# Optimization experiments

Hardware: AMD Instinct MI355X
Metric: run time of the kernel (lower is better)

## Reference

```python
import jax, jax.numpy as jnp
import numpy as np

N_EMBD = 256
HEAD_SIZE = 64


def setup_inputs() -> dict:
    key = jax.random.key(0)
    ks = jax.random.split(key, 6)
    B, T = 4, 4096
    x = jax.random.normal(ks[0], (B, T, N_EMBD), dtype=jnp.float32)
    s = 1.0 / np.sqrt(N_EMBD)
    Wk = jax.random.normal(ks[1], (N_EMBD, HEAD_SIZE), dtype=jnp.float32) * s
    bk = jax.random.normal(ks[2], (HEAD_SIZE,), dtype=jnp.float32) * s
    Wq = jax.random.normal(ks[3], (N_EMBD, HEAD_SIZE), dtype=jnp.float32) * s
    bq = jax.random.normal(ks[4], (HEAD_SIZE,), dtype=jnp.float32) * s
    Wv = jax.random.normal(ks[5], (N_EMBD, HEAD_SIZE), dtype=jnp.float32) * s
    return {"x": x, "Wk": Wk, "bk": bk, "Wq": Wq, "bq": bq, "Wv": Wv}


def reference(x, Wk, bk, Wq, bq, Wv):
    # x: [B, T, C] with C = n_embd = 256
    C = x.shape[-1]
    k = x @ Wk + bk          # [B, T, H]
    q = x @ Wq + bq          # [B, T, H]
    v = x @ Wv               # [B, T, H] (no bias)
    # NOTE: original scales by C**-0.5 (n_embd), not head_size**-0.5
    scale = jnp.asarray(C, x.dtype) ** -0.5
    wei = jnp.einsum("bth,bsh->bts", q, k) * scale   # [B, T, T]
    wei = jax.nn.softmax(wei, axis=-1)
    # dropout on attention weights is identity in eval mode
    out = jnp.einsum("bts,bsh->bth", wei, v)         # [B, T, H]
    return out
```

## Files before the change

### kernel.cpp

```cpp
#include <hip/hip_runtime.h>
#include <stdint.h>

#define QK_SCALE 0.09016844005555021f

typedef short short8 __attribute__((ext_vector_type(8)));
typedef float f32x4 __attribute__((ext_vector_type(4)));

static __device__ __forceinline__ unsigned short f2bf(float f){
  unsigned u = __builtin_bit_cast(unsigned, f);
  u += 0x7fffu + ((u >> 16) & 1u);
  return (unsigned short)(u >> 16);
}
static __device__ __forceinline__ float fexp2(float x){
  float r; asm("v_exp_f32 %0, %1" : "=v"(r) : "v"(x)); return r;
}
static __device__ __forceinline__ unsigned cvtpk(float lo, float hi){
  unsigned r; asm("v_cvt_pk_bf16_f32 %0, %1, %2" : "=v"(r) : "v"(lo), "v"(hi));
  return r;
}

__global__ __launch_bounds__(256) void pack_w_k(const float* __restrict__ Wk,
    const float* __restrict__ Wq, const float* __restrict__ Wv,
    unsigned short* __restrict__ wt){
  int j = blockIdx.x >> 6;
  int n = blockIdx.x & 63;
  int k = threadIdx.x;
  const float* W = (j==0) ? Wk : ((j==1) ? Wq : Wv);
  float s = (j==1) ? QK_SCALE : 1.0f;
  wt[j*16384 + n*256 + k] = f2bf(W[k*64 + n] * s);
}

__global__ __launch_bounds__(256) void qkv_proj_k(const float* __restrict__ x,
    const float* __restrict__ bk, const float* __restrict__ bq,
    const unsigned short* __restrict__ wt,
    unsigned short* __restrict__ qw, unsigned short* __restrict__ kw,
    unsigned short* __restrict__ vtw){
  __shared__ __align__(16) unsigned char xl[8192];
  __shared__ __align__(16) unsigned short vb[16*72];
  const int tid = threadIdx.x;
  const int r0 = blockIdx.x << 4;

  #pragma unroll
  for (int i=0;i<4;++i){
    int f4 = tid + (i<<8);
    float4 v = ((const float4*)x)[((size_t)r0<<6) + f4];
    int row = f4 >> 6;
    int byt = ((row<<9) + ((f4&63)<<3)) ^ ((row&7)<<4);
    uint2 pk; pk.x = cvtpk(v.x, v.y); pk.y = cvtpk(v.z, v.w);
    *(uint2*)(xl + byt) = pk;
  }
  __syncthreads();

  const int l = tid & 63, w = tid >> 6, g = l >> 4, c = l & 15;
  const int jn0 = w * 3;
  f32x4 acc[3];
  #pragma unroll
  for (int i=0;i<3;++i) acc[i] = (f32x4){0.f,0.f,0.f,0.f};

  #pragma unroll
  for (int kk=0;kk<8;++kk){
    short8 a = *(const short8*)(xl + (((c<<9) + (kk<<6) + (g<<4)) ^ ((c&7)<<4)));
    #pragma unroll
    for (int u=0;u<3;++u){
      int jn = jn0 + u, j = jn>>2, n = jn&3;
      short8 bf = *(const short8*)(wt + (size_t)j*16384 + (((n<<4)+c)<<8) + (kk<<5) + (g<<3));
      acc[u] = __builtin_amdgcn_mfma_f32_16x16x32_bf16(a, bf, acc[u], 0, 0, 0);
    }
  }

  #pragma unroll
  for (int u=0;u<3;++u){
    int jn = jn0 + u, j = jn>>2, n = jn&3;
    if (j == 0){
      float bK = bk[(n<<4)+c];
      #pragma unroll
      for (int r=0;r<4;++r)
        kw[((size_t)(r0 + (g<<2) + r)<<6) + (n<<4) + c] = f2bf(acc[u][r] + bK);
    } else if (j == 1){
      float bQ = bq[(n<<4)+c] * QK_SCALE;
      #pragma unroll
      for (int r=0;r<4;++r)
        qw[((size_t)(r0 + (g<<2) + r)<<6) + (n<<4) + c] = f2bf(acc[u][r] + bQ);
    } else {
      #pragma unroll
      for (int r=0;r<4;++r)
        vb[((g<<2)+r)*72 + (n<<4) + c] = f2bf(acc[u][r]);
    }
  }
  __syncthreads();
  int d = tid >> 2, tq = (tid & 3) << 2;
  unsigned s0 = vb[(tq+0)*72 + d], s1 = vb[(tq+1)*72 + d];
  unsigned s2 = vb[(tq+2)*72 + d], s3 = vb[(tq+3)*72 + d];
  uint2 pk; pk.x = s0 | (s1<<16); pk.y = s2 | (s3<<16);
  int b = r0 >> 12, t0 = r0 & 4095;
  *(uint2*)(vtw + (((size_t)(b<<6) + d)<<12) + t0 + tq) = pk;
}

__global__ __launch_bounds__(256) void attn_k(
    const unsigned short* __restrict__ qw, const unsigned short* __restrict__ kw,
    const unsigned short* __restrict__ vtw,
    float* __restrict__ opart, float* __restrict__ mpart, float* __restrict__ lpart){
  __shared__ __align__(16) unsigned char kl[16384];
  __shared__ __align__(16) unsigned char vl[16384];
  const int tid = threadIdx.x;
  const int l = tid & 63, w = tid >> 6, g = l >> 4, c = l & 15;
  const int qb = blockIdx.x, split = blockIdx.y;
  const int b = qb >> 5, tq0 = (qb & 31) << 7;
  const int kt0 = split << 3;

  short8 qa[2][2];
  #pragma unroll
  for (int mt=0;mt<2;++mt)
    #pragma unroll
    for (int kk=0;kk<2;++kk)
      qa[mt][kk] = *(const short8*)(qw +
        ((size_t)((b<<12) + tq0 + (w<<5) + (mt<<4) + c)<<6) + (kk<<5) + (g<<3));

  f32x4 o[2][4];
  float mrow[2] = {-1e30f, -1e30f}, lrow[2] = {0.f, 0.f};
  #pragma unroll
  for (int mt=0;mt<2;++mt)
    #pragma unroll
    for (int df=0;df<4;++df) o[mt][df] = (f32x4){0.f,0.f,0.f,0.f};

  const int srow = tid >> 3;
  const int scol = tid & 7;
  const int offA = ((scol>>2)<<6) + ((scol&1)<<5) + (((scol>>1)&1)<<3);
  const int offB = offA + 16;

  uint4 rk[2], rv[2];
  #define LOADT(kt) { \
    _Pragma("unroll") \
    for (int u=0;u<2;++u){ \
      int row = srow + (u<<5); \
      rk[u] = *(const uint4*)(kw + ((size_t)((b<<12) + ((kt)<<6) + row)<<6) + (scol<<3)); \
      rv[u] = *(const uint4*)(vtw + (((size_t)((b<<6) + row))<<12) + ((kt)<<6) + (scol<<3)); \
    } }
  #define STORET(buf) { \
    _Pragma("unroll") \
    for (int u=0;u<2;++u){ \
      int row = srow + (u<<5); \
      *(uint4*)(kl + ((buf)<<13) + (((row<<7)+(scol<<4)) ^ ((row&7)<<4))) = rk[u]; \
      unsigned char* vbase = vl + ((buf)<<13) + (row<<7); \
      int sz = (row&7)<<4; \
      uint2 t0_; t0_.x = rv[u].x; t0_.y = rv[u].y; \
      uint2 t1_; t1_.x = rv[u].z; t1_.y = rv[u].w; \
      *(uint2*)(vbase + (offA ^ sz)) = t0_; \
      *(uint2*)(vbase + (offB ^ sz)) = t1_; \
    } }

  LOADT(kt0); STORET(0);
  __syncthreads();

  for (int it=0; it<8; ++it){
    const int buf = it & 1;
    if (it < 7) LOADT(kt0 + it + 1);
    const unsigned char* kb_ = kl + (buf<<13);
    const unsigned char* vb_ = vl + (buf<<13);

    f32x4 s[2][4];
    #pragma unroll
    for (int mt=0;mt<2;++mt)
      #pragma unroll
      for (int n=0;n<4;++n) s[mt][n] = (f32x4){0.f,0.f,0.f,0.f};
    __builtin_amdgcn_s_setprio(1);
    #pragma unroll
    for (int kk=0;kk<2;++kk){
      #pragma unroll
      for (int n=0;n<4;++n){
        int rowk = (n<<4) + c;
        short8 ka = *(const short8*)(kb_ + (((rowk<<7) + (kk<<6) + (g<<4)) ^ ((rowk&7)<<4)));
        s[0][n] = __builtin_amdgcn_mfma_f32_16x16x32_bf16(ka, qa[0][kk], s[0][n], 0,0,0);
        s[1][n] = __builtin_amdgcn_mfma_f32_16x16x32_bf16(ka, qa[1][kk], s[1][n], 0,0,0);
      }
    }
    __builtin_amdgcn_s_setprio(0);

    short8 pb[2][2];
    #pragma unroll
    for (int mt=0;mt<2;++mt){
      float a0 = fmaxf(fmaxf(s[mt][0][0], s[mt][0][1]), fmaxf(s[mt][0][2], s[mt][0][3]));
      float a1 = fmaxf(fmaxf(s[mt][1][0], s[mt][1][1]), fmaxf(s[mt][1][2], s[mt][1][3]));
      float a2 = fmaxf(fmaxf(s[mt][2][0], s[mt][2][1]), fmaxf(s[mt][2][2], s[mt][2][3]));
      float a3 = fmaxf(fmaxf(s[mt][3][0], s[mt][3][1]), fmaxf(s[mt][3][2], s[mt][3][3]));
      float t0 = fmaxf(fmaxf(a0,a1), fmaxf(a2,a3));
      t0 = fmaxf(t0, __shfl_xor(t0, 16));
      t0 = fmaxf(t0, __shfl_xor(t0, 32));
      float mo = mrow[mt];
      if (!__all(t0 <= mo + 8.f)){
        float mn = fmaxf(mo, t0);
        float al = fexp2(mo - mn);
        mrow[mt] = mn; lrow[mt] *= al;
        #pragma unroll
        for (int df=0;df<4;++df){
          o[mt][df][0]*=al; o[mt][df][1]*=al; o[mt][df][2]*=al; o[mt][df][3]*=al;
        }
      }
      float m = mrow[mt];
      #pragma unroll
      for (int n=0;n<4;++n)
        #pragma unroll
        for (int r=0;r<4;++r) s[mt][n][r] = fexp2(s[mt][n][r] - m);
      float p0 = (s[mt][0][0]+s[mt][0][1]) + (s[mt][0][2]+s[mt][0][3]);
      float p1 = (s[mt][1][0]+s[mt][1][1]) + (s[mt][1][2]+s[mt][1][3]);
      float p2 = (s[mt][2][0]+s[mt][2][1]) + (s[mt][2][2]+s[mt][2][3]);
      float p3 = (s[mt][3][0]+s[mt][3][1]) + (s[mt][3][2]+s[mt][3][3]);
      lrow[mt] += (p0+p1) + (p2+p3);
      #pragma unroll
      for (int kk=0;kk<2;++kk){
        uint4 pw;
        pw.x = cvtpk(s[mt][2*kk][0],   s[mt][2*kk][1]);
        pw.y = cvtpk(s[mt][2*kk][2],   s[mt][2*kk][3]);
        pw.z = cvtpk(s[mt][2*kk+1][0], s[mt][2*kk+1][1]);
        pw.w = cvtpk(s[mt][2*kk+1][2], s[mt][2*kk+1][3]);
        pb[mt][kk] = __builtin_bit_cast(short8, pw);
      }
    }

    __builtin_amdgcn_s_setprio(1);
    #pragma unroll
    for (int kk=0;kk<2;++kk){
      #pragma unroll
      for (int df=0;df<4;++df){
        int rowd = (df<<4) + c;
        short8 va = *(const short8*)(vb_ + (((rowd<<7) + (kk<<6) + (g<<4)) ^ ((rowd&7)<<4)));
        o[0][df] = __builtin_amdgcn_mfma_f32_16x16x32_bf16(va, pb[0][kk], o[0][df], 0,0,0);
        o[1][df] = __builtin_amdgcn_mfma_f32_16x16x32_bf16(va, pb[1][kk], o[1][df], 0,0,0);
      }
    }
    __builtin_amdgcn_s_setprio(0);

    if (it < 7) STORET(buf^1);
    __syncthreads();
  }

  #pragma unroll
  for (int mt=0;mt<2;++mt){
    float ls = lrow[mt];
    ls += __shfl_xor(ls, 16);
    ls += __shfl_xor(ls, 32);
    int grow = (b<<12) + tq0 + (w<<5) + (mt<<4) + c;
    if (l < 16){
      mpart[(split<<14) + grow] = mrow[mt];
      lpart[(split<<14) + grow] = ls;
    }
    #pragma unroll
    for (int df=0;df<4;++df)
      *(f32x4*)(opart + ((size_t)split<<20) + ((size_t)grow<<6) + (df<<4) + (g<<2)) = o[mt][df];
  }
}

__global__ __launch_bounds__(256) void combine_k(const float* __restrict__ opart,
    const float* __restrict__ mpart, const float* __restrict__ lpart,
    float* __restrict__ out){
  int idx4 = blockIdx.x*256 + threadIdx.x;
  int row = idx4 >> 4;
  float mm = -1e30f;
  #pragma unroll
  for (int sp=0;sp<8;++sp) mm = fmaxf(mm, mpart[(sp<<14) + row]);
  f32x4 num = (f32x4){0.f,0.f,0.f,0.f};
  float den = 0.f;
  #pragma unroll
  for (int sp=0;sp<8;++sp){
    float a = fexp2(mpart[(sp<<14) + row] - mm);
    den += lpart[(sp<<14) + row] * a;
    f32x4 v = *(const f32x4*)(opart + ((size_t)sp<<20) + ((size_t)idx4<<2));
    num[0]+=v[0]*a; num[1]+=v[1]*a; num[2]+=v[2]*a; num[3]+=v[3]*a;
  }
  float inv = 1.0f / den;
  f32x4 r; r[0]=num[0]*inv; r[1]=num[1]*inv; r[2]=num[2]*inv; r[3]=num[3]*inv;
  *(f32x4*)(out + ((size_t)idx4<<2)) = r;
}

extern "C" void kernel_launch(void* const* d_in, const int* in_sizes, int n_in,
                              void* d_out, int out_size, void* d_ws, size_t ws_size,
                              hipStream_t stream){
  const float* x  = (const float*)d_in[0];
  const float* Wk = (const float*)d_in[1];
  const float* bk = (const float*)d_in[2];
  const float* Wq = (const float*)d_in[3];
  const float* bq = (const float*)d_in[4];
  const float* Wv = (const float*)d_in[5];
  unsigned char* ws = (unsigned char*)d_ws;
  unsigned short* wt  = (unsigned short*)(ws);
  unsigned short* qw  = (unsigned short*)(ws + 131072);
  unsigned short* kw  = (unsigned short*)(ws + 131072 + 2097152);
  unsigned short* vtw = (unsigned short*)(ws + 131072 + 2u*2097152);
  const size_t base = 131072 + 3u*2097152;
  float* opart = (float*)(ws + base);
  float* mpart = (float*)(ws + base + 8u*4194304u);
  float* lpart = (float*)(ws + base + 8u*4194304u + 524288u);
  float* out = (float*)d_out;

  hipLaunchKernelGGL(pack_w_k,   dim3(192),    dim3(256), 0, stream, Wk, Wq, Wv, wt);
  hipLaunchKernelGGL(qkv_proj_k, dim3(1024),   dim3(256), 0, stream, x, bk, bq, wt, qw, kw, vtw);
  hipLaunchKernelGGL(attn_k,     dim3(128, 8), dim3(256), 0, stream, qw, kw, vtw, opart, mpart, lpart);
  hipLaunchKernelGGL(combine_k,  dim3(1024),   dim3(256), 0, stream, opart, mpart, lpart, out);
}
```

Measured before the change: 126.2 us.

## Drop LDS staging in attention; load K and permuted V^T directly from global

The attention kernel no longer stages K and V tiles through double-buffered shared memory with a barrier per iteration. Each wave now loads its MFMA operands straight from global memory, relying on L2/L1 for reuse across the four waves. To support this, the projection kernel writes V^T in a pre-permuted column order that matches the MFMA fragment layout, so each lane's short8 load is contiguous. This removes the LDS writes, the swizzle arithmetic and the __syncthreads calls. In exchange every wave reissues global loads for the same K/V data, and there is no explicit prefetch, so global latency is exposed inside the loop.

```diff
diff --git a/kernel.cpp b/kernel.cpp
--- a/kernel.cpp
+++ b/kernel.cpp
@@ -93,15 +93,15 @@
   unsigned s2 = vb[(tq+2)*72 + d], s3 = vb[(tq+3)*72 + d];
   uint2 pk; pk.x = s0 | (s1<<16); pk.y = s2 | (s3<<16);
   int b = r0 >> 12, t0 = r0 & 4095;
-  *(uint2*)(vtw + (((size_t)(b<<6) + d)<<12) + t0 + tq) = pk;
+  int kk_ = (t0>>5)&1, hi_ = (t0>>4)&1;
+  int dst = (t0 & ~63) + (kk_<<5) + ((tid&3)<<3) + (hi_<<2);
+  *(uint2*)(vtw + (((size_t)(b<<6) + d)<<12) + dst) = pk;
 }
 
 __global__ __launch_bounds__(256) void attn_k(
     const unsigned short* __restrict__ qw, const unsigned short* __restrict__ kw,
-    const unsigned short* __restrict__ vtw,
+    const unsigned short* __restrict__ vtwp,
     float* __restrict__ opart, float* __restrict__ mpart, float* __restrict__ lpart){
-  __shared__ __align__(16) unsigned char kl[16384];
-  __shared__ __align__(16) unsigned char vl[16384];
   const int tid = threadIdx.x;
   const int l = tid & 63, w = tid >> 6, g = l >> 4, c = l & 15;
   const int qb = blockIdx.x, split = blockIdx.y;
@@ -123,40 +123,17 @@
     #pragma unroll
     for (int df=0;df<4;++df) o[mt][df] = (f32x4){0.f,0.f,0.f,0.f};
 
-  const int srow = tid >> 3;
-  const int scol = tid & 7;
-  const int offA = ((scol>>2)<<6) + ((scol&1)<<5) + (((scol>>1)&1)<<3);
-  const int offB = offA + 16;
-
-  uint4 rk[2], rv[2];
-  #define LOADT(kt) { \
-    _Pragma("unroll") \
-    for (int u=0;u<2;++u){ \
-      int row = srow + (u<<5); \
-      rk[u] = *(const uint4*)(kw + ((size_t)((b<<12) + ((kt)<<6) + row)<<6) + (scol<<3)); \
-      rv[u] = *(const uint4*)(vtw + (((size_t)((b<<6) + row))<<12) + ((kt)<<6) + (scol<<3)); \
-    } }
-  #define STORET(buf) { \
-    _Pragma("unroll") \
-    for (int u=0;u<2;++u){ \
-      int row = srow + (u<<5); \
-      *(uint4*)(kl + ((buf)<<13) + (((row<<7)+(scol<<4)) ^ ((row&7)<<4))) = rk[u]; \
-      unsigned char* vbase = vl + ((buf)<<13) + (row<<7); \
-      int sz = (row&7)<<4; \
-      uint2 t0_; t0_.x = rv[u].x; t0_.y = rv[u].y; \
-      uint2 t1_; t1_.x = rv[u].z; t1_.y = rv[u].w; \
-      *(uint2*)(vbase + (offA ^ sz)) = t0_; \
-      *(uint2*)(vbase + (offB ^ sz)) = t1_; \
-    } }
-
-  LOADT(kt0); STORET(0);
-  __syncthreads();
-
+  #pragma unroll 1
   for (int it=0; it<8; ++it){
-    const int buf = it & 1;
-    if (it < 7) LOADT(kt0 + it + 1);
-    const unsigned char* kb_ = kl + (buf<<13);
-    const unsigned char* vb_ = vl + (buf<<13);
+    const int kt = kt0 + it;
+
+    short8 ka[2][4];
+    #pragma unroll
+    for (int kk=0;kk<2;++kk)
+      #pragma unroll
+      for (int n=0;n<4;++n)
+        ka[kk][n] = *(const short8*)(kw +
+          ((size_t)((b<<12) + (kt<<6) + (n<<4) + c)<<6) + (kk<<5) + (g<<3));
 
     f32x4 s[2][4];
     #pragma unroll
@@ -168,10 +145,8 @@
     for (int kk=0;kk<2;++kk){
       #pragma unroll
       for (int n=0;n<4;++n){
-        int rowk = (n<<4) + c;
-        short8 ka = *(const short8*)(kb_ + (((rowk<<7) + (kk<<6) + (g<<4)) ^ ((rowk&7)<<4)));
-        s[0][n] = __builtin_amdgcn_mfma_f32_16x16x32_bf16(ka, qa[0][kk], s[0][n], 0,0,0);
-        s[1][n] = __builtin_amdgcn_mfma_f32_16x16x32_bf16(ka, qa[1][kk], s[1][n], 0,0,0);
+        s[0][n] = __builtin_amdgcn_mfma_f32_16x16x32_bf16(ka[kk][n], qa[0][kk], s[0][n], 0,0,0);
+        s[1][n] = __builtin_amdgcn_mfma_f32_16x16x32_bf16(ka[kk][n], qa[1][kk], s[1][n], 0,0,0);
       }
     }
     __builtin_amdgcn_s_setprio(0);
@@ -222,16 +197,13 @@
     for (int kk=0;kk<2;++kk){
       #pragma unroll
       for (int df=0;df<4;++df){
-        int rowd = (df<<4) + c;
-        short8 va = *(const short8*)(vb_ + (((rowd<<7) + (kk<<6) + (g<<4)) ^ ((rowd&7)<<4)));
+        short8 va = *(const short8*)(vtwp +
+          (((size_t)((b<<6) + (df<<4) + c))<<12) + (kt<<6) + (kk<<5) + (g<<3));
         o[0][df] = __builtin_amdgcn_mfma_f32_16x16x32_bf16(va, pb[0][kk], o[0][df], 0,0,0);
         o[1][df] = __builtin_amdgcn_mfma_f32_16x16x32_bf16(va, pb[1][kk], o[1][df], 0,0,0);
       }
     }
     __builtin_amdgcn_s_setprio(0);
-
-    if (it < 7) STORET(buf^1);
-    __syncthreads();
   }
 
   #pragma unroll
```

New measurement: 157.5 us. 24.8% more time.
